# Kernel tuning notes

Hardware: AMD Instinct MI355X
Metric: run time of the kernel (lower is better)

The kernel has to match this reference:

```python
import jax, jax.numpy as jnp
import numpy as np

B, QH, QW = 16, 64, 64
KH, KW = 64, 64
H, D, DK, K, S = 8, 256, 32, 4, 1


def setup_inputs() -> dict:
    key = jax.random.key(0)
    ks = jax.random.split(key, 16)
    def lin(i, din, dout, wscale=1.0):
        w = jax.random.normal(ks[i], (din, dout), jnp.float32) * (wscale / np.sqrt(din))
        b = jax.random.normal(ks[i + 1], (dout,), jnp.float32) * 0.02
        return w, b
    Wq, bq = lin(0, D, D)
    Wb, bb = lin(2, D, D)
    Wk, bk = lin(4, D, D)
    Woff, boff = lin(6, D, 2 * H * K * S, wscale=0.1)  # small offsets keep samples near ref point
    WA, bA = lin(8, D, H * K * S)
    Wm, bm = lin(10, D, D)
    return dict(
        query=jax.random.normal(ks[12], (B, QH, QW, D), jnp.float32),
        keys=jax.random.normal(ks[13], (B, KH, KW, D), jnp.float32),
        ref_point=jax.random.uniform(ks[14], (B, QH, QW, 2), jnp.float32),
        src_query=jax.random.normal(ks[15], (B, QH, QW, D), jnp.float32),
        Wq=Wq, bq=bq, Wb=Wb, bb=bb, Wk=Wk, bk=bk,
        Woff=Woff, boff=boff, WA=WA, bA=bA, Wm=Wm, bm=bm)


def _bilinear_zeros(img, px, py):
    # img [N, Hs, Ws, C]; px, py pixel coords [N, K, QH, QW]
    # Matches torch F.grid_sample(mode='bilinear', padding_mode='zeros'):
    # each out-of-bounds corner contributes zero.
    N, Hs, Ws, _ = img.shape
    x0 = jnp.floor(px); y0 = jnp.floor(py)
    wx1 = px - x0; wy1 = py - y0
    n = jnp.arange(N)[:, None, None, None]
    def corner(xf, yf, w):
        xi = xf.astype(jnp.int32); yi = yf.astype(jnp.int32)
        valid = (xi >= 0) & (xi < Ws) & (yi >= 0) & (yi < Hs)
        v = img[n, jnp.clip(yi, 0, Hs - 1), jnp.clip(xi, 0, Ws - 1)]
        return v * (w * valid)[..., None]
    return (corner(x0, y0, (1 - wx1) * (1 - wy1)) + corner(x0 + 1, y0, wx1 * (1 - wy1))
            + corner(x0, y0 + 1, (1 - wx1) * wy1) + corner(x0 + 1, y0 + 1, wx1 * wy1))


def reference(query, keys, ref_point, src_query, Wq, bq, Wb, bb, Wk, bk,
              Woff, boff, WA, bA, Wm, bm):
    _ = query @ Wq + bq  # q_proj output is computed but unused in the original forward
    sq = src_query @ Wb + bb
    off = (sq @ Woff + boff).reshape(B, QH, QW, H, S, K, 2)
    off = off.transpose(0, 3, 4, 5, 1, 2, 6).reshape(B * H, S, K, QH, QW, 2)
    A = jax.nn.softmax((sq @ WA + bA).reshape(B, QH, QW, H, S * K), axis=-1)
    A = A.transpose(0, 3, 1, 2, 4).reshape(B * H, QH, QW, S, K)
    # k_proj on the (single-scale) key feature map -> per-head maps [B*H, KH, KW, DK]
    kf = (keys @ Wk + bk).reshape(B, KH, KW, H, DK).transpose(0, 3, 1, 2, 4).reshape(B * H, KH, KW, DK)
    # restore_scale then torch .repeat(h,1,1,1): flat index n -> batch n % B (faithful to original)
    rr = ref_point * jnp.array([KW - 1, KH - 1], jnp.float32)
    rr = jnp.tile(rr, (H, 1, 1, 1))  # [B*H, QH, QW, 2]
    samples = []
    for l in range(S):
        pts = rr[:, None] + off[:, l]                 # [B*H, K, QH, QW, 2]
        vgx = 2.0 * pts[..., 0] / max(KW - 1, 1) - 1.0
        vgy = 2.0 * pts[..., 1] / max(KH - 1, 1) - 1.0
        px = ((vgx + 1.0) * KW - 1.0) / 2.0           # grid_sample align_corners=False unnormalize
        py = ((vgy + 1.0) * KH - 1.0) / 2.0
        samples.append(_bilinear_zeros(kf, px, py))   # [B*H, K, QH, QW, DK]
    samp = jnp.stack(samples, axis=1)                 # [B*H, S, K, QH, QW, DK]
    feat = jnp.einsum('nskhwd,nhwsk->nhwd', samp, A)  # weighted sum over scales*points
    feat = feat.reshape(B, H, QH, QW, DK).transpose(0, 2, 3, 1, 4).reshape(B, QH, QW, D)
    return feat @ Wm + bm
```

## Files before the change

### kernel.cpp

```cpp
#include <hip/hip_runtime.h>
#include <hip/hip_bf16.h>

using bf16 = __hip_bfloat16;
typedef short bf16x8 __attribute__((ext_vector_type(8)));
typedef short s16x4 __attribute__((ext_vector_type(4)));
typedef float f32x4 __attribute__((ext_vector_type(4)));
typedef unsigned int u32x4 __attribute__((ext_vector_type(4)));

#define DD 256
#define MTOT 65536

static __device__ __forceinline__ short f2bs(float f) {
    bf16 h = __float2bfloat16(f);
    return *reinterpret_cast<short*>(&h);
}

static __device__ __forceinline__ void gll16(const void* g, void* l) {
    __builtin_amdgcn_global_load_lds(
        (const __attribute__((address_space(1))) unsigned int*)g,
        (__attribute__((address_space(3))) unsigned int*)l, 16, 0, 0);
}

static __device__ __forceinline__ int swz_idx(int n, int k) {
    return n * 256 + ((((k >> 3) ^ (n & 7)) << 3) | (k & 7));
}

__global__ __launch_bounds__(256) void k_setup(
    const float* __restrict__ Wk, const float* __restrict__ Wm,
    bf16* __restrict__ WkT, bf16* __restrict__ WmT,
    const float* __restrict__ Wb, const float* __restrict__ bb,
    const float* __restrict__ Woff, const float* __restrict__ boff,
    const float* __restrict__ WA, const float* __restrict__ bA,
    bf16* __restrict__ WCt, float* __restrict__ bc)
{
    __shared__ float colw[256];
    __shared__ float red[256];
    int bid = blockIdx.x, t = threadIdx.x;
    if (bid < 512) {
        int idx = bid * 256 + t;
        int which = idx >> 16, e = idx & 65535;
        int i = e >> 8, j = e & 255;
        const float* src = which == 0 ? Wk : Wm;
        bf16*        dst = which == 0 ? WkT : WmT;
        dst[swz_idx(j, i)] = __float2bfloat16(src[e]);
        return;
    }
    int j = bid - 512;
    float cw = (j < 64) ? Woff[t * 64 + j] : WA[t * 32 + (j - 64)];
    colw[t] = cw;
    red[t] = bb[t] * cw;
    __syncthreads();
    float v = 0.f;
    const float* wbrow = Wb + (size_t)t * 256;
#pragma unroll 8
    for (int i = 0; i < 256; ++i) v += wbrow[i] * colw[i];
    WCt[swz_idx(j, t)] = __float2bfloat16(v);
    for (int s = 128; s > 0; s >>= 1) {
        __syncthreads();
        if (t < s) red[t] += red[t + s];
    }
    if (t == 0) bc[j] = red[0] + ((j < 64) ? boff[j] : bA[j - 64]);
}

template <int NTW, int NCOLS>
static __device__ __forceinline__ void gemm_lds4(
    const float* __restrict__ Av, const bf16* __restrict__ BTswz,
    char* __restrict__ Bsc, char* __restrict__ As,
    int row0, int tid, f32x4 (&acc)[2][NTW])
{
    const int wave = tid >> 6, lane = tid & 63;
    const int rg = wave >> 1, cg = wave & 1;
    const int rsub = lane & 15, kg = lane >> 4;
    constexpr int SB = NCOLS / 32;
    constexpr int BBYTES = NCOLS * 64 * 2;
    const int arow_l = lane >> 4;
    const int kb  = (lane & 15) * 4;
    const int g_l = (lane & 15) >> 1;
    const int sub = (lane & 15) & 1;

    f32x4 areg[4];
    auto loadA = [&](int s) {
#pragma unroll
        for (int c = 0; c < 4; ++c) {
            int row = wave * 16 + c * 4 + arow_l;
            areg[c] = *(const f32x4*)(Av + (size_t)(row0 + row) * DD + s * 64 + kb);
        }
    };
    auto writeA = [&](int buf) {
#pragma unroll
        for (int c = 0; c < 4; ++c) {
            int row = wave * 16 + c * 4 + arow_l;
            s16x4 p;
#pragma unroll
            for (int e = 0; e < 4; ++e) p[e] = f2bs(areg[c][e]);
            *(s16x4*)(As + buf * 8192 + row * 128 + ((g_l ^ (row & 7)) << 4) + sub * 8) = p;
        }
    };
    auto stageB = [&](int s, int buf) {
#pragma unroll
        for (int i = 0; i < SB; ++i) {
            int cc = wave * SB + i;
            int i16 = cc * 64 + lane;
            int n = i16 >> 3, lg = i16 & 7;
            gll16(BTswz + (size_t)n * 256 + s * 64 + lg * 8,
                  Bsc + buf * BBYTES + (size_t)i16 * 16);
        }
    };

    loadA(0);
    asm volatile("s_waitcnt vmcnt(0)" ::: "memory");
    writeA(0);
    stageB(0, 0);
    __builtin_amdgcn_sched_barrier(0);
    loadA(1);
    asm volatile("s_waitcnt vmcnt(0)" ::: "memory");
    asm volatile("s_waitcnt lgkmcnt(0)" ::: "memory");
    __builtin_amdgcn_s_barrier();

    int cur = 0;
#pragma unroll
    for (int s = 0; s < 4; ++s) {
        if (s < 3) {
            writeA(cur ^ 1);
            stageB(s + 1, cur ^ 1);
            __builtin_amdgcn_sched_barrier(0);
            if (s < 2) loadA(s + 2);
            __builtin_amdgcn_sched_barrier(0);
        }
#pragma unroll
        for (int kkl = 0; kkl < 2; ++kkl) {
            bf16x8 afr[2];
#pragma unroll
            for (int st = 0; st < 2; ++st) {
                int row = rg * 32 + st * 16 + rsub;
                int g = kkl * 4 + kg;
                afr[st] = *(const bf16x8*)(As + cur * 8192 + row * 128 + ((g ^ (row & 7)) << 4));
            }
            int lg = kkl * 4 + kg;
#pragma unroll
            for (int nt = 0; nt < NTW; ++nt) {
                int n = cg * (NTW * 16) + nt * 16 + rsub;
                bf16x8 b = *(const bf16x8*)(Bsc + cur * BBYTES + (size_t)n * 128 + ((lg ^ (n & 7)) << 4));
                acc[0][nt] = __builtin_amdgcn_mfma_f32_16x16x32_bf16(afr[0], b, acc[0][nt], 0, 0, 0);
                acc[1][nt] = __builtin_amdgcn_mfma_f32_16x16x32_bf16(afr[1], b, acc[1][nt], 0, 0, 0);
            }
        }
        asm volatile("s_waitcnt vmcnt(0) lgkmcnt(0)" ::: "memory");
        __builtin_amdgcn_s_barrier();
        cur ^= 1;
    }
}

template <int NTW, int NCOLS>
static __device__ __forceinline__ void gemm_lds5(
    const bf16* __restrict__ Av, const bf16* __restrict__ BTswz,
    char* __restrict__ Bsc, char* __restrict__ As,
    int row0, int tid, f32x4 (&acc)[2][NTW])
{
    const int wave = tid >> 6, lane = tid & 63;
    const int rg = wave >> 1, cg = wave & 1;
    const int rsub = lane & 15, kg = lane >> 4;
    constexpr int SB = NCOLS / 32;
    constexpr int BBYTES = NCOLS * 64 * 2;

    auto stageB = [&](int s, int buf) {
#pragma unroll
        for (int i = 0; i < SB; ++i) {
            int cc = wave * SB + i;
            int i16 = cc * 64 + lane;
            int n = i16 >> 3, lg = i16 & 7;
            gll16(BTswz + (size_t)n * 256 + s * 64 + lg * 8,
                  Bsc + buf * BBYTES + (size_t)i16 * 16);
        }
    };
    auto stageA = [&](int s, int buf) {
#pragma unroll
        for (int i = 0; i < 2; ++i) {
            int cc = wave * 2 + i;
            int row = cc * 8 + (lane >> 3);
            int g = (lane & 7) ^ (row & 7);
            gll16(Av + (size_t)(row0 + row) * DD + s * 64 + g * 8,
                  As + (size_t)buf * 8192 + cc * 1024 + lane * 16);
        }
    };

    stageB(0, 0);
    stageA(0, 0);
    asm volatile("s_waitcnt vmcnt(0)" ::: "memory");
    __builtin_amdgcn_s_barrier();

    int cur = 0;
#pragma unroll
    for (int s = 0; s < 4; ++s) {
        if (s < 3) {
            stageB(s + 1, cur ^ 1);
            stageA(s + 1, cur ^ 1);
            __builtin_amdgcn_sched_barrier(0);
        }
#pragma unroll
        for (int kkl = 0; kkl < 2; ++kkl) {
            bf16x8 afr[2];
#pragma unroll
            for (int st = 0; st < 2; ++st) {
                int row = rg * 32 + st * 16 + rsub;
                int g = kkl * 4 + kg;
                afr[st] = *(const bf16x8*)(As + cur * 8192 + row * 128 + ((g ^ (row & 7)) << 4));
            }
            int lg = kkl * 4 + kg;
#pragma unroll
            for (int nt = 0; nt < NTW; ++nt) {
                int n = cg * (NTW * 16) + nt * 16 + rsub;
                bf16x8 b = *(const bf16x8*)(Bsc + cur * BBYTES + (size_t)n * 128 + ((lg ^ (n & 7)) << 4));
                acc[0][nt] = __builtin_amdgcn_mfma_f32_16x16x32_bf16(afr[0], b, acc[0][nt], 0, 0, 0);
                acc[1][nt] = __builtin_amdgcn_mfma_f32_16x16x32_bf16(afr[1], b, acc[1][nt], 0, 0, 0);
            }
        }
        asm volatile("s_waitcnt vmcnt(0) lgkmcnt(0)" ::: "memory");
        __builtin_amdgcn_s_barrier();
        cur ^= 1;
    }
}

__global__ __launch_bounds__(256) void k_offA(
    const float* __restrict__ src, const bf16* __restrict__ WCt, const float* __restrict__ bc,
    float* __restrict__ off_ws, float* __restrict__ A_ws)
{
    __shared__ __align__(16) char Bsc[2 * 12288];
    __shared__ __align__(16) char As[2 * 8192];
    int tid = threadIdx.x, lane = tid & 63, wave = tid >> 6;
    int row0 = blockIdx.x * 64;
    f32x4 acc[2][3] = {};
    gemm_lds4<3, 96>(src, WCt, Bsc, As, row0, tid, acc);
    int col = lane & 15;
    int jbase = (wave & 1) * 48;
    int rb = row0 + (wave >> 1) * 32 + ((lane >> 4) << 2);
#pragma unroll
    for (int mt = 0; mt < 2; ++mt) {
#pragma unroll
        for (int nt = 0; nt < 3; ++nt) {
            int j = jbase + nt * 16 + col;
            if (j < 64) {
                float bias = bc[j];
#pragma unroll
                for (int r = 0; r < 4; ++r) {
                    int m = rb + mt * 16 + r;
                    off_ws[(size_t)m * 64 + j] = acc[mt][nt][r] + bias;
                }
            } else {
                int ac = j - 64;
                float bias = bc[j];
#pragma unroll
                for (int r = 0; r < 4; ++r) {
                    int m = rb + mt * 16 + r;
                    float v  = acc[mt][nt][r] + bias;
                    float mx = fmaxf(v, __shfl_xor(v, 1));
                    mx       = fmaxf(mx, __shfl_xor(mx, 2));
                    float e  = __expf(v - mx);
                    float su = e + __shfl_xor(e, 1);
                    su      += __shfl_xor(su, 2);
                    A_ws[(size_t)m * 32 + ac] = e / su;
                }
            }
        }
    }
}

__global__ __launch_bounds__(256) void k_gemm_kf(
    const float* __restrict__ keys, const bf16* __restrict__ WkT,
    const float* __restrict__ bk, bf16* __restrict__ kf)
{
    __shared__ __align__(16) char Bsc[2 * 32768];
    __shared__ __align__(16) char As[2 * 8192];
    int tid = threadIdx.x, lane = tid & 63, wave = tid >> 6;
    int row0 = blockIdx.x * 64;
    f32x4 acc[2][8] = {};
    gemm_lds4<8, 256>(keys, WkT, Bsc, As, row0, tid, acc);
    int col = lane & 15;
    int jbase = (wave & 1) * 128;
    int rb = row0 + (wave >> 1) * 32 + ((lane >> 4) << 2);
#pragma unroll
    for (int mt = 0; mt < 2; ++mt)
#pragma unroll
        for (int nt = 0; nt < 8; ++nt) {
            int j = jbase + nt * 16 + col;
            float bias = bk[j];
#pragma unroll
            for (int r = 0; r < 4; ++r) {
                int m = rb + mt * 16 + r;
                size_t dst = (((size_t)(m >> 12) * 8 + (j >> 5)) * 4096 + (m & 4095)) * 32 + (j & 31);
                kf[dst] = __float2bfloat16(acc[mt][nt][r] + bias);
            }
        }
}

__global__ __launch_bounds__(256) void k_sample(
    const float* __restrict__ ref_point, const float* __restrict__ off_ws,
    const float* __restrict__ A_ws, const bf16* __restrict__ kf,
    bf16* __restrict__ feat)
{
    int bid = blockIdx.x;
    int xcd = bid & 7, within = bid >> 3;
    int b = xcd * 2 + (within >> 9);
    int pixblk = within & 511;
    int t  = threadIdx.x;
    int q  = t >> 5;
    int h  = (t >> 2) & 7;
    int cg = t & 3;
    int m  = (b << 12) + pixblk * 8 + q;
    int pix = m & 4095;
    int rbatch = (b * 8 + h) & 15;
    const float* rp = ref_point + ((size_t)rbatch * 4096 + pix) * 2;
    float rx = rp[0] * 63.0f;
    float ry = rp[1] * 63.0f;
    const bf16* kfh = kf + ((size_t)(b * 8 + h) * 4096) * 32 + cg * 8;
    f32x4 o0 = *(const f32x4*)(off_ws + (size_t)m * 64 + h * 8);
    f32x4 o1 = *(const f32x4*)(off_ws + (size_t)m * 64 + h * 8 + 4);
    f32x4 av = *(const f32x4*)(A_ws  + (size_t)m * 32 + h * 4);
    float acc[8] = {};
#pragma unroll
    for (int k = 0; k < 4; ++k) {
        float ox = (k < 2) ? o0[2 * k] : o1[2 * k - 4];
        float oy = (k < 2) ? o0[2 * k + 1] : o1[2 * k - 3];
        float a  = av[k];
        float px = (rx + ox) * (64.0f / 63.0f) - 0.5f;
        float py = (ry + oy) * (64.0f / 63.0f) - 0.5f;
        float x0 = floorf(px), y0 = floorf(py);
        float wx1 = px - x0, wy1 = py - y0;
        int xi = (int)x0, yi = (int)y0;
        float ax0 = (1.f - wx1) * ((xi     >= 0 && xi     < 64) ? 1.f : 0.f);
        float ax1 = wx1         * ((xi + 1 >= 0 && xi + 1 < 64) ? 1.f : 0.f);
        float ay0 = (1.f - wy1) * ((yi     >= 0 && yi     < 64) ? a : 0.f);
        float ay1 = wy1         * ((yi + 1 >= 0 && yi + 1 < 64) ? a : 0.f);
        int xc0 = min(max(xi, 0), 63),      xc1 = min(max(xi + 1, 0), 63);
        int yc0 = min(max(yi, 0), 63) * 64, yc1 = min(max(yi + 1, 0), 63) * 64;
        float w00 = ax0 * ay0, w01 = ax1 * ay0, w10 = ax0 * ay1, w11 = ax1 * ay1;
        bf16x8 v00 = *(const bf16x8*)(kfh + (yc0 + xc0) * 32);
        bf16x8 v01 = *(const bf16x8*)(kfh + (yc0 + xc1) * 32);
        bf16x8 v10 = *(const bf16x8*)(kfh + (yc1 + xc0) * 32);
        bf16x8 v11 = *(const bf16x8*)(kfh + (yc1 + xc1) * 32);
        u32x4 u00 = __builtin_bit_cast(u32x4, v00);
        u32x4 u01 = __builtin_bit_cast(u32x4, v01);
        u32x4 u10 = __builtin_bit_cast(u32x4, v10);
        u32x4 u11 = __builtin_bit_cast(u32x4, v11);
#pragma unroll
        for (int d = 0; d < 4; ++d) {
            acc[2 * d]     += w00 * __uint_as_float(u00[d] << 16)
                            + w01 * __uint_as_float(u01[d] << 16)
                            + w10 * __uint_as_float(u10[d] << 16)
                            + w11 * __uint_as_float(u11[d] << 16);
            acc[2 * d + 1] += w00 * __uint_as_float(u00[d] & 0xffff0000u)
                            + w01 * __uint_as_float(u01[d] & 0xffff0000u)
                            + w10 * __uint_as_float(u10[d] & 0xffff0000u)
                            + w11 * __uint_as_float(u11[d] & 0xffff0000u);
        }
    }
    bf16x8 o;
#pragma unroll
    for (int e = 0; e < 8; ++e) o[e] = f2bs(acc[e]);
    *(bf16x8*)(feat + (size_t)m * DD + h * 32 + cg * 8) = o;
}

__global__ __launch_bounds__(256) void k_gemm_out(
    const bf16* __restrict__ feat, const bf16* __restrict__ WmT,
    const float* __restrict__ bm, float* __restrict__ out)
{
    __shared__ __align__(16) char Bsc[2 * 32768];
    __shared__ __align__(16) char As[2 * 8192];
    int tid = threadIdx.x, lane = tid & 63, wave = tid >> 6;
    int row0 = blockIdx.x * 64;
    f32x4 acc[2][8] = {};
    gemm_lds5<8, 256>(feat, WmT, Bsc, As, row0, tid, acc);
    int col = lane & 15;
    int jbase = (wave & 1) * 128;
    int rb = row0 + (wave >> 1) * 32 + ((lane >> 4) << 2);
#pragma unroll
    for (int mt = 0; mt < 2; ++mt)
#pragma unroll
        for (int nt = 0; nt < 8; ++nt) {
            int j = jbase + nt * 16 + col;
            float bias = bm[j];
#pragma unroll
            for (int r = 0; r < 4; ++r)
                out[(size_t)(rb + mt * 16 + r) * DD + j] =
                    acc[mt][nt][r] + bias;
        }
}

extern "C" void kernel_launch(void* const* d_in, const int* in_sizes, int n_in,
                              void* d_out, int out_size, void* d_ws, size_t ws_size,
                              hipStream_t stream)
{
    (void)in_sizes; (void)n_in; (void)out_size; (void)ws_size;
    const float* keys = (const float*)d_in[1];
    const float* refp = (const float*)d_in[2];
    const float* srcq = (const float*)d_in[3];
    const float* Wb   = (const float*)d_in[6];
    const float* bb   = (const float*)d_in[7];
    const float* Wk   = (const float*)d_in[8];
    const float* bk   = (const float*)d_in[9];
    const float* Woff = (const float*)d_in[10];
    const float* boff = (const float*)d_in[11];
    const float* WA   = (const float*)d_in[12];
    const float* bA   = (const float*)d_in[13];
    const float* Wm   = (const float*)d_in[14];
    const float* bm   = (const float*)d_in[15];

    char* ws = (char*)d_ws;
    bf16*  WkT    = (bf16*)(ws + 0);
    bf16*  WmT    = (bf16*)(ws + 131072);
    bf16*  WCt    = (bf16*)(ws + 262144);
    float* bc     = (float*)(ws + 311296);
    bf16*  kf_ws  = (bf16*)(ws + 442368 + 33554432ull);
    bf16*  feat_ws= (bf16*)(ws + 442368 + 2ull * 33554432ull);
    float* off_ws = (float*)(ws + 442368 + 3ull * 33554432ull);
    float* A_ws   = (float*)(ws + 442368 + 3ull * 33554432ull + 16777216ull);

    float* out = (float*)d_out;

    k_setup    <<<608, 256, 0, stream>>>(Wk, Wm, WkT, WmT, Wb, bb, Woff, boff, WA, bA, WCt, bc);
    k_offA     <<<1024, 256, 0, stream>>>(srcq, WCt, bc, off_ws, A_ws);
    k_gemm_kf  <<<1024, 256, 0, stream>>>(keys, WkT, bk, kf_ws);
    k_sample   <<<8192, 256, 0, stream>>>(refp, off_ws, A_ws, kf_ws, feat_ws);
    k_gemm_out <<<1024, 256, 0, stream>>>(feat_ws, WmT, bm, out);
}
```

Measured before the change: 114.4 us.

## Fuse offset/attention GEMM with bilinear sampling, keeping offsets in LDS

Merges the offset/attention-weight projection kernel into the sampling kernel. Each 64-row block now writes its offsets and softmax weights to shared memory and samples its own 64 query pixels from there. This removes the global round trip for off_ws/A_ws (about 24 MB) and one kernel launch. In exchange, sampling parallelism drops from 8192 blocks to 1024 blocks, each looping over 8 pixel groups. The XCD-aware block-to-batch mapping is also gone, which may hurt L2 locality of the kf reads.

```diff
diff --git a/kernel.cpp b/kernel.cpp
--- a/kernel.cpp
+++ b/kernel.cpp
@@ -221,50 +221,6 @@
     }
 }
 
-__global__ __launch_bounds__(256) void k_offA(
-    const float* __restrict__ src, const bf16* __restrict__ WCt, const float* __restrict__ bc,
-    float* __restrict__ off_ws, float* __restrict__ A_ws)
-{
-    __shared__ __align__(16) char Bsc[2 * 12288];
-    __shared__ __align__(16) char As[2 * 8192];
-    int tid = threadIdx.x, lane = tid & 63, wave = tid >> 6;
-    int row0 = blockIdx.x * 64;
-    f32x4 acc[2][3] = {};
-    gemm_lds4<3, 96>(src, WCt, Bsc, As, row0, tid, acc);
-    int col = lane & 15;
-    int jbase = (wave & 1) * 48;
-    int rb = row0 + (wave >> 1) * 32 + ((lane >> 4) << 2);
-#pragma unroll
-    for (int mt = 0; mt < 2; ++mt) {
-#pragma unroll
-        for (int nt = 0; nt < 3; ++nt) {
-            int j = jbase + nt * 16 + col;
-            if (j < 64) {
-                float bias = bc[j];
-#pragma unroll
-                for (int r = 0; r < 4; ++r) {
-                    int m = rb + mt * 16 + r;
-                    off_ws[(size_t)m * 64 + j] = acc[mt][nt][r] + bias;
-                }
-            } else {
-                int ac = j - 64;
-                float bias = bc[j];
-#pragma unroll
-                for (int r = 0; r < 4; ++r) {
-                    int m = rb + mt * 16 + r;
-                    float v  = acc[mt][nt][r] + bias;
-                    float mx = fmaxf(v, __shfl_xor(v, 1));
-                    mx       = fmaxf(mx, __shfl_xor(mx, 2));
-                    float e  = __expf(v - mx);
-                    float su = e + __shfl_xor(e, 1);
-                    su      += __shfl_xor(su, 2);
-                    A_ws[(size_t)m * 32 + ac] = e / su;
-                }
-            }
-        }
-    }
-}
-
 __global__ __launch_bounds__(256) void k_gemm_kf(
     const float* __restrict__ keys, const bf16* __restrict__ WkT,
     const float* __restrict__ bk, bf16* __restrict__ kf)
@@ -293,71 +249,111 @@
         }
 }
 
-__global__ __launch_bounds__(256) void k_sample(
-    const float* __restrict__ ref_point, const float* __restrict__ off_ws,
-    const float* __restrict__ A_ws, const bf16* __restrict__ kf,
+__global__ __launch_bounds__(256) void k_offA_sample(
+    const float* __restrict__ src, const bf16* __restrict__ WCt, const float* __restrict__ bc,
+    const float* __restrict__ ref_point, const bf16* __restrict__ kf,
     bf16* __restrict__ feat)
 {
-    int bid = blockIdx.x;
-    int xcd = bid & 7, within = bid >> 3;
-    int b = xcd * 2 + (within >> 9);
-    int pixblk = within & 511;
-    int t  = threadIdx.x;
-    int q  = t >> 5;
-    int h  = (t >> 2) & 7;
-    int cg = t & 3;
-    int m  = (b << 12) + pixblk * 8 + q;
-    int pix = m & 4095;
+    __shared__ __align__(16) char smem[40960];
+    char* Bsc = smem;
+    char* As  = smem + 24576;
+    int tid = threadIdx.x, lane = tid & 63, wave = tid >> 6;
+    int row0 = blockIdx.x * 64;
+    f32x4 acc[2][3] = {};
+    gemm_lds4<3, 96>(src, WCt, Bsc, As, row0, tid, acc);
+
+    float* off_l = (float*)smem;
+    float* A_l   = (float*)(smem + 16384);
+    {
+        int col = lane & 15;
+        int jbase = (wave & 1) * 48;
+        int lrb = (wave >> 1) * 32 + ((lane >> 4) << 2);
+#pragma unroll
+        for (int mt = 0; mt < 2; ++mt) {
+#pragma unroll
+            for (int nt = 0; nt < 3; ++nt) {
+                int j = jbase + nt * 16 + col;
+                if (j < 64) {
+                    float bias = bc[j];
+#pragma unroll
+                    for (int r = 0; r < 4; ++r)
+                        off_l[(lrb + mt * 16 + r) * 64 + j] = acc[mt][nt][r] + bias;
+                } else {
+                    int ac = j - 64;
+                    float bias = bc[j];
+#pragma unroll
+                    for (int r = 0; r < 4; ++r) {
+                        float v  = acc[mt][nt][r] + bias;
+                        float mx = fmaxf(v, __shfl_xor(v, 1));
+                        mx       = fmaxf(mx, __shfl_xor(mx, 2));
+                        float e  = __expf(v - mx);
+                        float su = e + __shfl_xor(e, 1);
+                        su      += __shfl_xor(su, 2);
+                        A_l[(lrb + mt * 16 + r) * 32 + ac] = e / su;
+                    }
+                }
+            }
+        }
+    }
+    __syncthreads();
+
+    int q  = tid >> 5;
+    int h  = (tid >> 2) & 7;
+    int cg = tid & 3;
+    int b  = row0 >> 12;
     int rbatch = (b * 8 + h) & 15;
-    const float* rp = ref_point + ((size_t)rbatch * 4096 + pix) * 2;
-    float rx = rp[0] * 63.0f;
-    float ry = rp[1] * 63.0f;
     const bf16* kfh = kf + ((size_t)(b * 8 + h) * 4096) * 32 + cg * 8;
-    f32x4 o0 = *(const f32x4*)(off_ws + (size_t)m * 64 + h * 8);
-    f32x4 o1 = *(const f32x4*)(off_ws + (size_t)m * 64 + h * 8 + 4);
-    f32x4 av = *(const f32x4*)(A_ws  + (size_t)m * 32 + h * 4);
-    float acc[8] = {};
-#pragma unroll
-    for (int k = 0; k < 4; ++k) {
-        float ox = (k < 2) ? o0[2 * k] : o1[2 * k - 4];
-        float oy = (k < 2) ? o0[2 * k + 1] : o1[2 * k - 3];
-        float a  = av[k];
-        float px = (rx + ox) * (64.0f / 63.0f) - 0.5f;
-        float py = (ry + oy) * (64.0f / 63.0f) - 0.5f;
-        float x0 = floorf(px), y0 = floorf(py);
-        float wx1 = px - x0, wy1 = py - y0;
-        int xi = (int)x0, yi = (int)y0;
-        float ax0 = (1.f - wx1) * ((xi     >= 0 && xi     < 64) ? 1.f : 0.f);
-        float ax1 = wx1         * ((xi + 1 >= 0 && xi + 1 < 64) ? 1.f : 0.f);
-        float ay0 = (1.f - wy1) * ((yi     >= 0 && yi     < 64) ? a : 0.f);
-        float ay1 = wy1         * ((yi + 1 >= 0 && yi + 1 < 64) ? a : 0.f);
-        int xc0 = min(max(xi, 0), 63),      xc1 = min(max(xi + 1, 0), 63);
-        int yc0 = min(max(yi, 0), 63) * 64, yc1 = min(max(yi + 1, 0), 63) * 64;
-        float w00 = ax0 * ay0, w01 = ax1 * ay0, w10 = ax0 * ay1, w11 = ax1 * ay1;
-        bf16x8 v00 = *(const bf16x8*)(kfh + (yc0 + xc0) * 32);
-        bf16x8 v01 = *(const bf16x8*)(kfh + (yc0 + xc1) * 32);
-        bf16x8 v10 = *(const bf16x8*)(kfh + (yc1 + xc0) * 32);
-        bf16x8 v11 = *(const bf16x8*)(kfh + (yc1 + xc1) * 32);
-        u32x4 u00 = __builtin_bit_cast(u32x4, v00);
-        u32x4 u01 = __builtin_bit_cast(u32x4, v01);
-        u32x4 u10 = __builtin_bit_cast(u32x4, v10);
-        u32x4 u11 = __builtin_bit_cast(u32x4, v11);
-#pragma unroll
-        for (int d = 0; d < 4; ++d) {
-            acc[2 * d]     += w00 * __uint_as_float(u00[d] << 16)
-                            + w01 * __uint_as_float(u01[d] << 16)
-                            + w10 * __uint_as_float(u10[d] << 16)
-                            + w11 * __uint_as_float(u11[d] << 16);
-            acc[2 * d + 1] += w00 * __uint_as_float(u00[d] & 0xffff0000u)
-                            + w01 * __uint_as_float(u01[d] & 0xffff0000u)
-                            + w10 * __uint_as_float(u10[d] & 0xffff0000u)
-                            + w11 * __uint_as_float(u11[d] & 0xffff0000u);
-        }
-    }
-    bf16x8 o;
-#pragma unroll
-    for (int e = 0; e < 8; ++e) o[e] = f2bs(acc[e]);
-    *(bf16x8*)(feat + (size_t)m * DD + h * 32 + cg * 8) = o;
+#pragma unroll 2
+    for (int qq = 0; qq < 8; ++qq) {
+        int lr = qq * 8 + q;
+        int m  = row0 + lr;
+        int pix = m & 4095;
+        const float* rp = ref_point + ((size_t)rbatch * 4096 + pix) * 2;
+        float rx = rp[0] * 63.0f;
+        float ry = rp[1] * 63.0f;
+        float acs[8] = {};
+#pragma unroll
+        for (int k = 0; k < 4; ++k) {
+            float ox = off_l[lr * 64 + (h * 4 + k) * 2];
+            float oy = off_l[lr * 64 + (h * 4 + k) * 2 + 1];
+            float a  = A_l[lr * 32 + h * 4 + k];
+            float px = (rx + ox) * (64.0f / 63.0f) - 0.5f;
+            float py = (ry + oy) * (64.0f / 63.0f) - 0.5f;
+            float x0 = floorf(px), y0 = floorf(py);
+            float wx1 = px - x0, wy1 = py - y0;
+            int xi = (int)x0, yi = (int)y0;
+            float ax0 = (1.f - wx1) * ((xi     >= 0 && xi     < 64) ? 1.f : 0.f);
+            float ax1 = wx1         * ((xi + 1 >= 0 && xi + 1 < 64) ? 1.f : 0.f);
+            float ay0 = (1.f - wy1) * ((yi     >= 0 && yi     < 64) ? a : 0.f);
+            float ay1 = wy1         * ((yi + 1 >= 0 && yi + 1 < 64) ? a : 0.f);
+            int xc0 = min(max(xi, 0), 63),      xc1 = min(max(xi + 1, 0), 63);
+            int yc0 = min(max(yi, 0), 63) * 64, yc1 = min(max(yi + 1, 0), 63) * 64;
+            float w00 = ax0 * ay0, w01 = ax1 * ay0, w10 = ax0 * ay1, w11 = ax1 * ay1;
+            bf16x8 v00 = *(const bf16x8*)(kfh + (yc0 + xc0) * 32);
+            bf16x8 v01 = *(const bf16x8*)(kfh + (yc0 + xc1) * 32);
+            bf16x8 v10 = *(const bf16x8*)(kfh + (yc1 + xc0) * 32);
+            bf16x8 v11 = *(const bf16x8*)(kfh + (yc1 + xc1) * 32);
+            u32x4 u00 = __builtin_bit_cast(u32x4, v00);
+            u32x4 u01 = __builtin_bit_cast(u32x4, v01);
+            u32x4 u10 = __builtin_bit_cast(u32x4, v10);
+            u32x4 u11 = __builtin_bit_cast(u32x4, v11);
+#pragma unroll
+            for (int d = 0; d < 4; ++d) {
+                acs[2 * d]     += w00 * __uint_as_float(u00[d] << 16)
+                                + w01 * __uint_as_float(u01[d] << 16)
+                                + w10 * __uint_as_float(u10[d] << 16)
+                                + w11 * __uint_as_float(u11[d] << 16);
+                acs[2 * d + 1] += w00 * __uint_as_float(u00[d] & 0xffff0000u)
+                                + w01 * __uint_as_float(u01[d] & 0xffff0000u)
+                                + w10 * __uint_as_float(u10[d] & 0xffff0000u)
+                                + w11 * __uint_as_float(u11[d] & 0xffff0000u);
+            }
+        }
+        bf16x8 o;
+#pragma unroll
+        for (int e = 0; e < 8; ++e) o[e] = f2bs(acs[e]);
+        *(bf16x8*)(feat + (size_t)m * DD + h * 32 + cg * 8) = o;
+    }
 }
 
 __global__ __launch_bounds__(256) void k_gemm_out(
@@ -412,14 +408,11 @@
     float* bc     = (float*)(ws + 311296);
     bf16*  kf_ws  = (bf16*)(ws + 442368 + 33554432ull);
     bf16*  feat_ws= (bf16*)(ws + 442368 + 2ull * 33554432ull);
-    float* off_ws = (float*)(ws + 442368 + 3ull * 33554432ull);
-    float* A_ws   = (float*)(ws + 442368 + 3ull * 33554432ull + 16777216ull);
 
     float* out = (float*)d_out;
 
-    k_setup    <<<608, 256, 0, stream>>>(Wk, Wm, WkT, WmT, Wb, bb, Woff, boff, WA, bA, WCt, bc);
-    k_offA     <<<1024, 256, 0, stream>>>(srcq, WCt, bc, off_ws, A_ws);
-    k_gemm_kf  <<<1024, 256, 0, stream>>>(keys, WkT, bk, kf_ws);
-    k_sample   <<<8192, 256, 0, stream>>>(refp, off_ws, A_ws, kf_ws, feat_ws);
-    k_gemm_out <<<1024, 256, 0, stream>>>(feat_ws, WmT, bm, out);
-}
+    k_setup      <<<608, 256, 0, stream>>>(Wk, Wm, WkT, WmT, Wb, bb, Woff, boff, WA, bA, WCt, bc);
+    k_gemm_kf    <<<1024, 256, 0, stream>>>(keys, WkT, bk, kf_ws);
+    k_offA_sample<<<1024, 256, 0, stream>>>(srcq, WCt, bc, refp, kf_ws, feat_ws);
+    k_gemm_out   <<<1024, 256, 0, stream>>>(feat_ws, WmT, bm, out);
+}
```

Result: slower. 120.7 us (+5.5%).
